# Performance work log

Hardware: AMD Instinct MI355X
Metric: run time of the kernel (lower is better)

## Reference

```python
import jax, jax.numpy as jnp
import numpy as np


def _find(parent, x):
    # chase parent pointers to the root (root = min-rank node of its component)
    return jax.lax.while_loop(lambda v: parent[v] != v, lambda v: parent[v], x)


def _pd0_single(fcol, src, dst):
    """0-dim persistence diagram for one filtration column.

    Semantics match TOGL.generate_persistence_diagram_dim0:
      - nodes are added in sorted order of fcol; birth(node) = its sorted rank
      - directed edge (u, v) merges components at step rank(v) iff rank(u) < rank(v)
      - elder rule: the component whose root has the larger rank dies
      - output row i = (birth=i, death) for the node of rank i (insertion order of
        the original dict is exactly rank order); death = inf for survivors.
    """
    n = fcol.shape[0]
    order = jnp.argsort(fcol)
    rank = jnp.zeros((n,), jnp.int32).at[order].set(jnp.arange(n, dtype=jnp.int32))
    a = rank[src]                      # rank-space endpoints
    b = rank[dst]
    valid = a < b                      # only edges whose source is already active fire
    w = jnp.where(valid, b, n)         # edge weight = step at which it fires
    perm = jnp.argsort(w)              # Kruskal order
    ea, eb, ev = a[perm], b[perm], valid[perm]

    def step(carry, e):
        parent, deaths = carry
        ia, ib, v = e
        ra = _find(parent, ia)
        rb = _find(parent, ib)
        merge = v & (ra != rb)
        elder = jnp.minimum(ra, rb)
        younger = jnp.maximum(ra, rb)
        deaths = deaths.at[younger].set(jnp.where(merge, ib.astype(deaths.dtype), deaths[younger]))
        parent = parent.at[younger].set(jnp.where(merge, elder, parent[younger]))
        # path compression at the two queried nodes
        parent = parent.at[ia].set(jnp.where(merge, elder, ra))
        parent = parent.at[ib].set(jnp.where(merge, elder, rb))
        return (parent, deaths), None

    parent0 = jnp.arange(n, dtype=jnp.int32)
    deaths0 = jnp.full((n,), jnp.inf, jnp.float32)
    (parent, deaths), _ = jax.lax.scan(step, (parent0, deaths0), (ea, eb, ev))
    births = jnp.arange(n, dtype=jnp.float32)
    return jnp.stack([births, deaths], axis=1)  # (n_nodes, 2)


def setup_inputs() -> dict:
    key = jax.random.key(0)
    k = jax.random.split(key, 6)
    N, F, H, NF, E = 20000, 1024, 2048, 4, 160000
    X = jax.random.normal(k[0], (N, F), jnp.float32)
    edge_index = jax.random.randint(k[1], (2, E), 0, N, jnp.int64)
    W1 = jax.random.normal(k[2], (F, H), jnp.float32) / np.sqrt(F)
    b1 = jax.random.normal(k[3], (H,), jnp.float32) * 0.01
    W2 = jax.random.normal(k[4], (H, NF), jnp.float32) / np.sqrt(H)
    b2 = jax.random.normal(k[5], (NF,), jnp.float32) * 0.01
    return {"X": X, "edge_index": edge_index, "W1": W1, "b1": b1, "W2": W2, "b2": b2}


def reference(X, edge_index, W1, b1, W2, b2):
    # filter_graph: Linear -> ReLU -> Linear
    filt = jnp.maximum(X @ W1 + b1, 0.0) @ W2 + b2            # (N, n_filtrations)
    src = edge_index[0].astype(jnp.int32)
    dst = edge_index[1].astype(jnp.int32)
    diagrams = jax.vmap(_pd0_single, in_axes=(1, None, None))(filt, src, dst)  # (NF, N, 2)
    return filt, diagrams
```

## Files before the change

### kernel.cpp

```cpp
#include <hip/hip_runtime.h>

typedef unsigned long long u64;
typedef unsigned int u32;
typedef unsigned short ushort_t;
typedef __attribute__((ext_vector_type(8))) short short8;
typedef __attribute__((ext_vector_type(4))) float fx4;

#define F_DIM 1024
#define H_DIM 2048
#define NFOUT 4
#define WS_W1T_OFF (1ull << 20)
#define WS_XS_OFF  (16ull << 20)
#define PB_BYTES   ((size_t)H_DIM * F_DIM * 2)

__device__ __forceinline__ ushort_t f2bf(float x)
{
    union { float f; u32 u; } c; c.f = x;
    u32 b = c.u;
    u32 r = b + 0x7FFFu + ((b >> 16) & 1u);
    return (ushort_t)(r >> 16);
}
__device__ __forceinline__ float bf2f(ushort_t h)
{
    union { u32 u; float f; } c; c.u = ((u32)h) << 16;
    return c.f;
}
__device__ __forceinline__ void split3(float x, ushort_t& u0, ushort_t& u1, ushort_t& u2)
{
    u0 = f2bf(x);
    float r1 = x - bf2f(u0);
    u1 = f2bf(r1);
    float r2 = r1 - bf2f(u1);
    u2 = f2bf(r2);
}

__device__ __forceinline__ void gload16(const void* g, void* l)
{
    __builtin_amdgcn_global_load_lds(
        (const __attribute__((address_space(1))) unsigned int*)g,
        (__attribute__((address_space(3))) unsigned int*)l, 16, 0, 0);
}

__global__ __launch_bounds__(256)
void k_w1split(const float* __restrict__ W1, ushort_t* __restrict__ w1t)
{
    __shared__ __align__(16) ushort_t LT[3][64][72];
    const int t = threadIdx.x;
    const int bk = blockIdx.x >> 5;
    const int bh = blockIdx.x & 31;
    const int k0 = bk * 64, h0 = bh * 64;
    const int kk = t >> 4, hb = (t & 15) * 4;
    #pragma unroll
    for (int j = 0; j < 4; j++) {
        int row = kk + j * 16;
        float4 v = *(const float4*)(W1 + (size_t)(k0 + row) * H_DIM + h0 + hb);
        float xs[4] = { v.x, v.y, v.z, v.w };
        #pragma unroll
        for (int c = 0; c < 4; c++) {
            ushort_t u0, u1, u2;
            split3(xs[c], u0, u1, u2);
            LT[0][hb + c][row] = u0;
            LT[1][hb + c][row] = u1;
            LT[2][hb + c][row] = u2;
        }
    }
    __syncthreads();
    const int hl = t >> 2, sg = t & 3;
    char* wb = (char*)w1t;
    const int hsw = (hl & 7) << 4;
    #pragma unroll
    for (int p = 0; p < 3; p++)
        #pragma unroll
        for (int q = 0; q < 2; q++) {
            int ks = sg * 16 + q * 8;
            *(short8*)(wb + (size_t)p * PB_BYTES + (size_t)(h0 + hl) * 2048
                       + bk * 128 + ((ks * 2) ^ hsw)) =
                *(const short8*)&LT[p][hl][ks];
        }
}

__global__ __launch_bounds__(256)
void k_xsplit(const float* __restrict__ X, ushort_t* __restrict__ xs,
              int N, int Npad)
{
    const int row = blockIdx.x;
    if (row >= N) return;
    const int t = threadIdx.x;
    float4 v = *(const float4*)(X + (size_t)row * F_DIM + t * 4);
    const int swz = (row & 7) << 4;
    const int off = ((t * 8) & ~127) | (((t * 8) & 127) ^ swz);
    const size_t PA = (size_t)Npad * 2048;
    char* base = (char*)xs + (size_t)row * 2048 + off;
    float in[4] = { v.x, v.y, v.z, v.w };
    ushort4 u0, u1, u2;
    ushort_t* p0 = (ushort_t*)&u0; ushort_t* p1 = (ushort_t*)&u1; ushort_t* p2 = (ushort_t*)&u2;
    #pragma unroll
    for (int j = 0; j < 4; j++) split3(in[j], p0[j], p1[j], p2[j]);
    *(ushort4*)(base)          = u0;
    *(ushort4*)(base + PA)     = u1;
    *(ushort4*)(base + 2 * PA) = u2;
}

__device__ __forceinline__ fx4 mfma16(short8 a, short8 b, fx4 c)
{
    return __builtin_amdgcn_mfma_f32_16x16x32_bf16(a, b, c, 0, 0, 0);
}

#define A4_BYTES (3 * 80 * 128)
#define B4_BYTES (3 * 256 * 128)
#define W24_OFF  (A4_BYTES + B4_BYTES)
#define SM4_BYTES (W24_OFF + 256 * 4 * 4)
#define HP4 260

__global__ __launch_bounds__(512, 1)
void k_filt_mfma4(const ushort_t* __restrict__ xs, const ushort_t* __restrict__ w1t,
                  const float* __restrict__ b1, const float* __restrict__ W2,
                  const float* __restrict__ b2, float* __restrict__ out,
                  int N, int Npad)
{
    extern __shared__ char smem[];
    char* Ac = smem;
    char* Bc = smem + A4_BYTES;
    float* W2s = (float*)(smem + W24_OFF);
    float* hid = (float*)smem;

    const int t = threadIdx.x;
    const int lane = t & 63;
    const int w = t >> 6;
    const int wc = w * 32;
    const int r0 = blockIdx.x * 80;
    const int l15 = lane & 15, l4 = lane >> 4;
    const int fsw = (l15 & 7) << 4;

    const char* xsb = (const char*)xs;
    const char* w1b = (const char*)w1t;
    const size_t PA = (size_t)Npad * 2048;
    const int laneoff = (lane >> 3) * 2048 + ((lane & 7) << 4);

    const int orow = t >> 2;
    const int onf  = t & 3;

    fx4 acc[5][2];
    #pragma unroll
    for (int i = 0; i < 5; i++)
        #pragma unroll
        for (int j = 0; j < 2; j++) acc[i][j] = (fx4)(0.f);
    float pacc = 0.f;

    for (int it = 0; it < 128; ++it) {
        const int hc = it >> 4, kc = it & 15;

        __syncthreads();

        for (int g = w; g < 126; g += 8) {
            char* ldsb; const char* src;
            if (g < 30) {
                const int p = g / 10, rg = g - p * 10;
                ldsb = Ac + p * 10240 + rg * 1024;
                src  = xsb + (size_t)p * PA + (size_t)(r0 + rg * 8) * 2048 + kc * 128;
            } else {
                const int gb = g - 30;
                const int p = gb >> 5, rg = gb & 31;
                ldsb = Bc + p * 32768 + rg * 1024;
                src  = w1b + (size_t)p * PB_BYTES + (size_t)(hc * 256 + rg * 8) * 2048 + kc * 128;
            }
            gload16(src + laneoff, ldsb);
        }
        if (kc == 0 && t < 256)
            *(float4*)&W2s[t * 4] = *(const float4*)(W2 + ((size_t)hc * 256 + t) * NFOUT);

        __syncthreads();

        #pragma unroll
        for (int sub = 0; sub < 2; ++sub) {
            const int kb = (sub * 64 + l4 * 16) ^ fsw;
            short8 b[2][3];
            #pragma unroll
            for (int cf = 0; cf < 2; ++cf) {
                const int hrow = wc + cf * 16 + l15;
                #pragma unroll
                for (int p = 0; p < 3; p++)
                    b[cf][p] = *(const short8*)(Bc + p * 32768 + hrow * 128 + kb);
            }
            #pragma unroll
            for (int rr = 0; rr < 5; ++rr) {
                const int row = rr * 16 + l15;
                short8 a0 = *(const short8*)(Ac + 0 * 10240 + row * 128 + kb);
                short8 a1 = *(const short8*)(Ac + 1 * 10240 + row * 128 + kb);
                short8 a2 = *(const short8*)(Ac + 2 * 10240 + row * 128 + kb);
                #pragma unroll
                for (int cf = 0; cf < 2; ++cf) {
                    fx4 c = acc[rr][cf];
                    c = mfma16(a0, b[cf][0], c);
                    c = mfma16(a0, b[cf][1], c);
                    c = mfma16(a1, b[cf][0], c);
                    c = mfma16(a0, b[cf][2], c);
                    c = mfma16(a1, b[cf][1], c);
                    c = mfma16(a2, b[cf][0], c);
                    acc[rr][cf] = c;
                }
            }
        }

        if (kc == 15) {
            __syncthreads();
            #pragma unroll
            for (int rr = 0; rr < 5; ++rr)
                #pragma unroll
                for (int cf = 0; cf < 2; ++cf) {
                    const int hl = wc + cf * 16 + l15;
                    const float bias1 = b1[hc * 256 + hl];
                    #pragma unroll
                    for (int g = 0; g < 4; g++) {
                        const int rl = rr * 16 + l4 * 4 + g;
                        hid[rl * HP4 + hl] = fmaxf(acc[rr][cf][g] + bias1, 0.f);
                    }
                    acc[rr][cf] = (fx4)(0.f);
                }
            __syncthreads();
            if (orow < 80) {
                const float* hp = hid + orow * HP4;
                #pragma unroll 16
                for (int j = 0; j < 256; j++)
                    pacc = fmaf(hp[j], W2s[j * 4 + onf], pacc);
            }
        }
    }

    if (orow < 80) {
        const int rg = r0 + orow;
        if (rg < N) out[(size_t)rg * NFOUT + onf] = pacc + b2[onf];
    }
}

#define AP_BYTES (3 * 128 * 128)
#define BP_BYTES (3 * 256 * 128)
#define W2_OFF   (AP_BYTES + BP_BYTES)
#define SM_BYTES (W2_OFF + 256 * 4 * 4)
#define HPITCH 260

__global__ __launch_bounds__(512, 2)
void k_filt_mfma3(const float* __restrict__ X, const ushort_t* __restrict__ w1t,
                  const float* __restrict__ b1, const float* __restrict__ W2,
                  const float* __restrict__ b2, float* __restrict__ out, int N)
{
    extern __shared__ char smem[];
    char* Ac = smem;
    char* Bc = smem + AP_BYTES;
    float* W2s = (float*)(smem + W2_OFF);
    float* hid = (float*)smem;

    const int t = threadIdx.x;
    const int lane = t & 63;
    const int w = t >> 6;
    const int wr = (w >> 2) * 64;
    const int wc = (w & 3) * 64;
    const int r0 = blockIdx.x * 128;
    const int l15 = lane & 15, l4 = lane >> 4;
    const int fsw = (l15 & 7) << 4;

    const int arow = t >> 2;
    const int aq   = (t & 3);
    const bool arow_ok = (r0 + arow) < N;
    const int brow = t >> 1;
    const int bseg = (t & 1) * 64;
    const int orow = t >> 2;
    const int onf  = t & 3;

    float Afl[16];
    short8 Bv[12];
    fx4 acc[4][4];
    float pacc = 0.f;
    #pragma unroll
    for (int i = 0; i < 4; i++)
        #pragma unroll
        for (int j = 0; j < 4; j++) acc[i][j] = (fx4)(0.f);

    {
        if (arow_ok) {
            #pragma unroll
            for (int q = 0; q < 4; q++) {
                float4 v = *(const float4*)(X + (size_t)(r0 + arow) * F_DIM + aq * 16 + q * 4);
                Afl[q * 4 + 0] = v.x; Afl[q * 4 + 1] = v.y;
                Afl[q * 4 + 2] = v.z; Afl[q * 4 + 3] = v.w;
            }
        } else {
            #pragma unroll
            for (int j = 0; j < 16; j++) Afl[j] = 0.f;
        }
        #pragma unroll
        for (int p = 0; p < 3; p++)
            #pragma unroll
            for (int q = 0; q < 4; q++)
                Bv[p * 4 + q] = *(const short8*)((const char*)w1t + (size_t)p * PB_BYTES
                                 + (size_t)brow * 2048 + bseg + q * 16);
    }

    for (int it = 0; it < 128; ++it) {
        const int hc = it >> 4, kc = it & 15;

        ushort_t s0[16], s1[16], s2[16];
        #pragma unroll
        for (int j = 0; j < 16; j++) split3(Afl[j], s0[j], s1[j], s2[j]);

        __syncthreads();

        {
            const int aswz = (arow & 7) << 4;
            #pragma unroll
            for (int p = 0; p < 3; p++) {
                const ushort_t* sp = (p == 0) ? s0 : (p == 1) ? s1 : s2;
                #pragma unroll
                for (int h = 0; h < 2; h++) {
                    short8 pk;
                    #pragma unroll
                    for (int i = 0; i < 8; i++) pk[i] = (short)sp[h * 8 + i];
                    *(short8*)(Ac + p * 16384 + arow * 128 + ((aq * 32 + h * 16) ^ aswz)) = pk;
                }
            }
            const int bswz = (brow & 7) << 4;
            #pragma unroll
            for (int p = 0; p < 3; p++)
                #pragma unroll
                for (int q = 0; q < 4; q++)
                    *(short8*)(Bc + p * 32768 + brow * 128 + ((bseg + q * 16) ^ bswz)) = Bv[p * 4 + q];
            if (kc == 0 && t < 256)
                *(float4*)&W2s[t * 4] = *(const float4*)(W2 + ((size_t)hc * 256 + t) * NFOUT);
        }

        if (it + 1 < 128) {
            const int hn = (it + 1) >> 4, kn = (it + 1) & 15;
            if (arow_ok) {
                #pragma unroll
                for (int q = 0; q < 4; q++) {
                    float4 v = *(const float4*)(X + (size_t)(r0 + arow) * F_DIM + kn * 64 + aq * 16 + q * 4);
                    Afl[q * 4 + 0] = v.x; Afl[q * 4 + 1] = v.y;
                    Afl[q * 4 + 2] = v.z; Afl[q * 4 + 3] = v.w;
                }
            }
            #pragma unroll
            for (int p = 0; p < 3; p++)
                #pragma unroll
                for (int q = 0; q < 4; q++)
                    Bv[p * 4 + q] = *(const short8*)((const char*)w1t + (size_t)p * PB_BYTES
                                     + (size_t)(hn * 256 + brow) * 2048 + kn * 128 + bseg + q * 16);
        }

        __syncthreads();

        #pragma unroll
        for (int sub = 0; sub < 2; ++sub) {
            const int kb = sub * 64 + l4 * 16;
            short8 b[4][3];
            #pragma unroll
            for (int cf = 0; cf < 4; ++cf) {
                const int hrow = wc + cf * 16 + l15;
                #pragma unroll
                for (int p = 0; p < 3; p++)
                    b[cf][p] = *(const short8*)(Bc + p * 32768 + hrow * 128 + (kb ^ fsw));
            }
            #pragma unroll
            for (int rr = 0; rr < 4; ++rr) {
                const int row = wr + rr * 16 + l15;
                short8 a0 = *(const short8*)(Ac + 0 * 16384 + row * 128 + (kb ^ fsw));
                short8 a1 = *(const short8*)(Ac + 1 * 16384 + row * 128 + (kb ^ fsw));
                short8 a2 = *(const short8*)(Ac + 2 * 16384 + row * 128 + (kb ^ fsw));
                #pragma unroll
                for (int cf = 0; cf < 4; ++cf) {
                    fx4 c = acc[rr][cf];
                    c = mfma16(a0, b[cf][0], c);
                    c = mfma16(a0, b[cf][1], c);
                    c = mfma16(a1, b[cf][0], c);
                    c = mfma16(a0, b[cf][2], c);
                    c = mfma16(a1, b[cf][1], c);
                    c = mfma16(a2, b[cf][0], c);
                    acc[rr][cf] = c;
                }
            }
        }

        if (kc == 15) {
            __syncthreads();
            #pragma unroll
            for (int rr = 0; rr < 4; ++rr)
                #pragma unroll
                for (int cf = 0; cf < 4; ++cf) {
                    const int hl = wc + cf * 16 + l15;
                    const float bias1 = b1[hc * 256 + hl];
                    #pragma unroll
                    for (int g = 0; g < 4; g++) {
                        const int rl = wr + rr * 16 + l4 * 4 + g;
                        hid[rl * HPITCH + hl] = fmaxf(acc[rr][cf][g] + bias1, 0.f);
                    }
                    acc[rr][cf] = (fx4)(0.f);
                }
            __syncthreads();
            {
                const float* hp = hid + orow * HPITCH;
                #pragma unroll 16
                for (int j = 0; j < 256; j++)
                    pacc = fmaf(hp[j], W2s[j * 4 + onf], pacc);
            }
        }
    }

    {
        const int rg = r0 + orow;
        if (rg < N) out[(size_t)rg * NFOUT + onf] = pacc + b2[onf];
    }
}

#define BM 64
#define BH 64
#define KCH 64
#define LROW 68

__global__ __launch_bounds__(256, 2)
void k_filt(const float* __restrict__ X, const float* __restrict__ W1,
            const float* __restrict__ b1, const float* __restrict__ W2,
            const float* __restrict__ b2, float* __restrict__ out, int N)
{
    __shared__ float Xs[KCH * LROW];
    __shared__ float Ws[KCH * LROW];
    __shared__ float W2s[BH * NFOUT];
    const int t = threadIdx.x;
    const int r0 = blockIdx.x * BM;
    const int tr = t >> 4, tc = t & 15;
    const int orow = t >> 2, onf = t & 3;
    float fchain = 0.0f;
    for (int hc = 0; hc < H_DIM; hc += BH) {
        float acc[4][4];
        #pragma unroll
        for (int i = 0; i < 4; i++)
            #pragma unroll
            for (int j = 0; j < 4; j++) acc[i][j] = 0.0f;
        for (int kc = 0; kc < F_DIM; kc += KCH) {
            {
                const int rowq = t >> 4, kkq = t & 15;
                float xv[4][4];
                #pragma unroll
                for (int j = 0; j < 4; j++) {
                    int r = r0 + rowq * 4 + j;
                    float4 v = (r < N) ? *(const float4*)(X + (size_t)r * F_DIM + kc + kkq * 4)
                                       : make_float4(0.f, 0.f, 0.f, 0.f);
                    xv[j][0] = v.x; xv[j][1] = v.y; xv[j][2] = v.z; xv[j][3] = v.w;
                }
                #pragma unroll
                for (int j = 0; j < 4; j++)
                    *(float4*)&Xs[(kkq * 4 + j) * LROW + rowq * 4] =
                        make_float4(xv[0][j], xv[1][j], xv[2][j], xv[3][j]);
            }
            {
                const int hq = t & 15;
                #pragma unroll
                for (int q = 0; q < 4; q++) {
                    int kk = (t >> 4) + q * 16;
                    *(float4*)&Ws[kk * LROW + hq * 4] =
                        *(const float4*)(W1 + (size_t)(kc + kk) * H_DIM + hc + hq * 4);
                }
            }
            __syncthreads();
            #pragma unroll 8
            for (int kk = 0; kk < KCH; kk++) {
                float4 xv = *(float4*)&Xs[kk * LROW + tr * 4];
                float4 wv = *(float4*)&Ws[kk * LROW + tc * 4];
                acc[0][0] = fmaf(xv.x, wv.x, acc[0][0]); acc[0][1] = fmaf(xv.x, wv.y, acc[0][1]);
                acc[0][2] = fmaf(xv.x, wv.z, acc[0][2]); acc[0][3] = fmaf(xv.x, wv.w, acc[0][3]);
                acc[1][0] = fmaf(xv.y, wv.x, acc[1][0]); acc[1][1] = fmaf(xv.y, wv.y, acc[1][1]);
                acc[1][2] = fmaf(xv.y, wv.z, acc[1][2]); acc[1][3] = fmaf(xv.y, wv.w, acc[1][3]);
                acc[2][0] = fmaf(xv.z, wv.x, acc[2][0]); acc[2][1] = fmaf(xv.z, wv.y, acc[2][1]);
                acc[2][2] = fmaf(xv.z, wv.z, acc[2][2]); acc[2][3] = fmaf(xv.z, wv.w, acc[2][3]);
                acc[3][0] = fmaf(xv.w, wv.x, acc[3][0]); acc[3][1] = fmaf(xv.w, wv.y, acc[3][1]);
                acc[3][2] = fmaf(xv.w, wv.z, acc[3][2]); acc[3][3] = fmaf(xv.w, wv.w, acc[3][3]);
            }
            __syncthreads();
        }
        {
            float4 bv = *(const float4*)(b1 + hc + tc * 4);
            #pragma unroll
            for (int i = 0; i < 4; i++) {
                float4 hv;
                hv.x = fmaxf(acc[i][0] + bv.x, 0.f);
                hv.y = fmaxf(acc[i][1] + bv.y, 0.f);
                hv.z = fmaxf(acc[i][2] + bv.z, 0.f);
                hv.w = fmaxf(acc[i][3] + bv.w, 0.f);
                *(float4*)&Ws[(tr * 4 + i) * LROW + tc * 4] = hv;
            }
            if (t < BH)
                *(float4*)&W2s[t * 4] = *(const float4*)(W2 + (size_t)(hc + t) * NFOUT);
        }
        __syncthreads();
        #pragma unroll 16
        for (int hh = 0; hh < BH; hh++)
            fchain = fmaf(Ws[orow * LROW + hh], W2s[hh * 4 + onf], fchain);
        __syncthreads();
    }
    {
        int r = r0 + orow;
        if (r < N) out[(size_t)r * NFOUT + onf] = fchain + b2[onf];
    }
}

__global__ void k_prep(u32* __restrict__ rank, int N)
{
    int g = blockIdx.x * blockDim.x + threadIdx.x;
    if (g < 4 * N) rank[g] = 0u;
}

#define JTILE 2048

__global__ __launch_bounds__(256)
void k_rank(const float* __restrict__ filt, u32* __restrict__ rank,
            int N, int nchunk)
{
    __shared__ float4 lds[JTILE];
    const int chunk = blockIdx.x % nchunk;
    const int jslice = blockIdx.x / nchunk;
    const int jt = jslice * JTILE;
    const int i = chunk * 256 + threadIdx.x;
    const bool iok = i < N;
    float4 vi = iok ? *(const float4*)(filt + (size_t)i * 4)
                    : make_float4(0.f, 0.f, 0.f, 0.f);
    for (int s = 0; s < JTILE; s += 256) {
        int j = jt + s + threadIdx.x;
        lds[s + threadIdx.x] = (j < N)
            ? *(const float4*)(filt + (size_t)j * 4)
            : make_float4(INFINITY, INFINITY, INFINITY, INFINITY);
    }
    __syncthreads();
    int c0 = 0, c1 = 0, c2 = 0, c3 = 0;
    #pragma unroll 4
    for (int jj = 0; jj < JTILE; jj++) {
        float4 vj = lds[jj];
        int j = jt + jj;
        bool jlt = j < i;
        c0 += (vj.x < vi.x) || (vj.x == vi.x && jlt);
        c1 += (vj.y < vi.y) || (vj.y == vi.y && jlt);
        c2 += (vj.z < vi.z) || (vj.z == vi.z && jlt);
        c3 += (vj.w < vi.w) || (vj.w == vi.w && jlt);
    }
    if (iok) {
        atomicAdd(&rank[0 * N + i], (u32)c0);
        atomicAdd(&rank[1 * N + i], (u32)c1);
        atomicAdd(&rank[2 * N + i], (u32)c2);
        atomicAdd(&rank[3 * N + i], (u32)c3);
    }
}

__device__ __forceinline__ u32 lds_aload(u32* p)
{
    return __hip_atomic_load(p, __ATOMIC_RELAXED, __HIP_MEMORY_SCOPE_WORKGROUP);
}

__device__ __forceinline__ u32 rep_walk32(u32* S, u32 u, u32 t, u32& sv_out)
{
    u32 sv = lds_aload(&S[u]);
    while ((sv >> 16) <= t) {
        u = sv & 0xFFFFu;
        sv = lds_aload(&S[u]);
    }
    sv_out = sv;
    return u;
}

__device__ void do_merge32(u32* S, u32 u, u32 v, u32 t)
{
    for (int guard = 0; guard < (1 << 22); guard++) {
        u32 svu, svv;
        u = rep_walk32(S, u, t, svu);
        v = rep_walk32(S, v, t, svv);
        if (u == v) return;
        if (u < v) { u32 tm = u; u = v; v = tm; u32 ts = svu; svu = svv; svv = ts; }
        u32 s = svu >> 16;
        if (s <= t) continue;
        u32 des = (t << 16) | v;
        u32 old = atomicCAS(&S[u], svu, des);
        if (old == svu) {
            if (s == 0xFFFFu) return;
            u = v; v = old & 0xFFFFu;
            t = s;
        }
    }
}

__global__ __launch_bounds__(1024, 1)
void k_merge4(const int* __restrict__ eidx, const u32* __restrict__ rank,
              float* __restrict__ dg, int N, int E)
{
    extern __shared__ u32 S[];
    const int f = blockIdx.x;
    const u32* rk = rank + (size_t)f * N;

    for (int u = threadIdx.x; u < N; u += blockDim.x)
        S[u] = (0xFFFFu << 16) | (u32)u;
    __syncthreads();

    for (int e = threadIdx.x; e < E; e += blockDim.x) {
        u32 a = rk[eidx[e]];
        u32 b = rk[eidx[E + e]];
        if (a < b) do_merge32(S, a, b, b);
    }
    __syncthreads();

    for (int r = threadIdx.x; r < N; r += blockDim.x) {
        u32 s = S[r] >> 16;
        float death = (s == 0xFFFFu) ? 3.0e38f : (float)s;
        dg[(size_t)f * N * 2 + (size_t)r * 2 + 0] = (float)r;
        dg[(size_t)f * N * 2 + (size_t)r * 2 + 1] = death;
    }
}

extern "C" void kernel_launch(void* const* d_in, const int* in_sizes, int n_in,
                              void* d_out, int out_size, void* d_ws, size_t ws_size,
                              hipStream_t stream)
{
    const float* X  = (const float*)d_in[0];
    const int*   EI = (const int*)d_in[1];
    const float* W1 = (const float*)d_in[2];
    const float* b1 = (const float*)d_in[3];
    const float* W2 = (const float*)d_in[4];
    const float* b2 = (const float*)d_in[5];
    const int N = in_sizes[0] / F_DIM;
    const int E = in_sizes[1] / 2;

    float* out = (float*)d_out;
    float* dg  = out + (size_t)N * NFOUT;
    u32* rank  = (u32*)d_ws;

    static bool attr_set = false;
    if (!attr_set) {
        (void)hipFuncSetAttribute((const void*)k_merge4,
                                  hipFuncAttributeMaxDynamicSharedMemorySize, 160 * 1024);
        (void)hipFuncSetAttribute((const void*)k_filt_mfma3,
                                  hipFuncAttributeMaxDynamicSharedMemorySize, 160 * 1024);
        (void)hipFuncSetAttribute((const void*)k_filt_mfma4,
                                  hipFuncAttributeMaxDynamicSharedMemorySize, 160 * 1024);
        attr_set = true;
    }

    k_prep<<<(4 * N + 255) / 256, 256, 0, stream>>>(rank, N);

    const int Npad = ((N + 79) / 80) * 80;
    const size_t need_w1t = WS_W1T_OFF + 3ull * PB_BYTES;
    const size_t need_xs  = WS_XS_OFF + 3ull * (size_t)Npad * 2048;

    if (ws_size >= need_xs) {
        ushort_t* w1t = (ushort_t*)((char*)d_ws + WS_W1T_OFF);
        ushort_t* xsp = (ushort_t*)((char*)d_ws + WS_XS_OFF);
        k_w1split<<<512, 256, 0, stream>>>(W1, w1t);
        k_xsplit<<<N, 256, 0, stream>>>(X, xsp, N, Npad);
        k_filt_mfma4<<<Npad / 80, 512, SM4_BYTES, stream>>>(xsp, w1t, b1, W2, b2, out, N, Npad);
    } else if (ws_size >= need_w1t) {
        ushort_t* w1t = (ushort_t*)((char*)d_ws + WS_W1T_OFF);
        k_w1split<<<512, 256, 0, stream>>>(W1, w1t);
        k_filt_mfma3<<<(N + 127) / 128, 512, SM_BYTES, stream>>>(X, w1t, b1, W2, b2, out, N);
    } else {
        k_filt<<<(N + BM - 1) / BM, 256, 0, stream>>>(X, W1, b1, W2, b2, out, N);
    }

    const int nchunk = (N + 255) / 256;
    const int njt    = (N + JTILE - 1) / JTILE;
    k_rank<<<nchunk * njt, 256, 0, stream>>>(out, rank, N, nchunk);
    k_merge4<<<4, 1024, (size_t)N * sizeof(u32), stream>>>(EI, rank, dg, N, E);
}
```

Before: 1.457 ms.

## Split K across wave pairs in filter GEMM and bucket merge edges by rank

The bf16x3 filter GEMM kernel now has each pair of waves split the K chunk in half, and each wave computes 64 hidden columns instead of 32. The two partial sums are reduced through LDS before bias and ReLU. Global-to-LDS load addresses are precomputed once outside the main loop, and the launch bound is raised to 2 blocks per CU. The union-find merge kernel now processes edges in 5 passes bucketed by death rank (b>>12), which adds repeated edge reads but may lower contention and deep find chains.

```diff
diff --git a/kernel.cpp b/kernel.cpp
--- a/kernel.cpp
+++ b/kernel.cpp
@@ -106,31 +106,33 @@
     return __builtin_amdgcn_mfma_f32_16x16x32_bf16(a, b, c, 0, 0, 0);
 }
 
-#define A4_BYTES (3 * 80 * 128)
-#define B4_BYTES (3 * 256 * 128)
-#define W24_OFF  (A4_BYTES + B4_BYTES)
-#define SM4_BYTES (W24_OFF + 256 * 4 * 4)
-#define HP4 260
-
-__global__ __launch_bounds__(512, 1)
-void k_filt_mfma4(const ushort_t* __restrict__ xs, const ushort_t* __restrict__ w1t,
+#define A5_BYTES (3 * 80 * 128)
+#define B5_BYTES (3 * 256 * 128)
+#define W25_OFF  (A5_BYTES + B5_BYTES)
+#define SM5_BYTES (W25_OFF + 256 * 4 * 4)
+#define HP5 260
+
+__global__ __launch_bounds__(512, 2)
+void k_filt_mfma5(const ushort_t* __restrict__ xs, const ushort_t* __restrict__ w1t,
                   const float* __restrict__ b1, const float* __restrict__ W2,
                   const float* __restrict__ b2, float* __restrict__ out,
                   int N, int Npad)
 {
     extern __shared__ char smem[];
     char* Ac = smem;
-    char* Bc = smem + A4_BYTES;
-    float* W2s = (float*)(smem + W24_OFF);
+    char* Bc = smem + A5_BYTES;
+    float* W2s = (float*)(smem + W25_OFF);
     float* hid = (float*)smem;
 
     const int t = threadIdx.x;
     const int lane = t & 63;
     const int w = t >> 6;
-    const int wc = w * 32;
+    const int ksub = w & 1;
+    const int wc = (w >> 1) * 64;
     const int r0 = blockIdx.x * 80;
     const int l15 = lane & 15, l4 = lane >> 4;
     const int fsw = (l15 & 7) << 4;
+    const int kb = (ksub * 64 + l4 * 16) ^ fsw;
 
     const char* xsb = (const char*)xs;
     const char* w1b = (const char*)w1t;
@@ -140,11 +142,31 @@
     const int orow = t >> 2;
     const int onf  = t & 3;
 
-    fx4 acc[5][2];
+    const char* srcb[16];
+    char* dstb[16];
+    bool isA[16];
+    #pragma unroll
+    for (int i = 0; i < 16; ++i) {
+        const int g = w + 8 * i;
+        if (g < 30) {
+            const int p = g / 10, rg = g - p * 10;
+            isA[i] = true;
+            dstb[i] = Ac + p * 10240 + rg * 1024;
+            srcb[i] = xsb + (size_t)p * PA + (size_t)(r0 + rg * 8) * 2048 + laneoff;
+        } else {
+            const int gb = g - 30;
+            const int p = gb >> 5, rg = gb & 31;
+            isA[i] = false;
+            dstb[i] = Bc + p * 32768 + rg * 1024;
+            srcb[i] = w1b + (size_t)p * PB_BYTES + (size_t)(rg * 8) * 2048 + laneoff;
+        }
+    }
+
+    fx4 acc[5][4];
     #pragma unroll
     for (int i = 0; i < 5; i++)
         #pragma unroll
-        for (int j = 0; j < 2; j++) acc[i][j] = (fx4)(0.f);
+        for (int j = 0; j < 4; j++) acc[i][j] = (fx4)(0.f);
     float pacc = 0.f;
 
     for (int it = 0; it < 128; ++it) {
@@ -152,35 +174,28 @@
 
         __syncthreads();
 
-        for (int g = w; g < 126; g += 8) {
-            char* ldsb; const char* src;
-            if (g < 30) {
-                const int p = g / 10, rg = g - p * 10;
-                ldsb = Ac + p * 10240 + rg * 1024;
-                src  = xsb + (size_t)p * PA + (size_t)(r0 + rg * 8) * 2048 + kc * 128;
-            } else {
-                const int gb = g - 30;
-                const int p = gb >> 5, rg = gb & 31;
-                ldsb = Bc + p * 32768 + rg * 1024;
-                src  = w1b + (size_t)p * PB_BYTES + (size_t)(hc * 256 + rg * 8) * 2048 + kc * 128;
-            }
-            gload16(src + laneoff, ldsb);
+        {
+            const size_t kcoff = (size_t)(kc * 128);
+            const size_t bcoff = (size_t)hc * 524288 + kcoff;
+            #pragma unroll
+            for (int i = 0; i < 16; ++i) {
+                if (i == 15 && w >= 6) continue;
+                gload16(srcb[i] + (isA[i] ? kcoff : bcoff), dstb[i]);
+            }
         }
         if (kc == 0 && t < 256)
             *(float4*)&W2s[t * 4] = *(const float4*)(W2 + ((size_t)hc * 256 + t) * NFOUT);
 
         __syncthreads();
 
-        #pragma unroll
-        for (int sub = 0; sub < 2; ++sub) {
-            const int kb = (sub * 64 + l4 * 16) ^ fsw;
-            short8 b[2][3];
-            #pragma unroll
-            for (int cf = 0; cf < 2; ++cf) {
+        {
+            short8 bfr[4][3];
+            #pragma unroll
+            for (int cf = 0; cf < 4; ++cf) {
                 const int hrow = wc + cf * 16 + l15;
                 #pragma unroll
                 for (int p = 0; p < 3; p++)
-                    b[cf][p] = *(const short8*)(Bc + p * 32768 + hrow * 128 + kb);
+                    bfr[cf][p] = *(const short8*)(Bc + p * 32768 + hrow * 128 + kb);
             }
             #pragma unroll
             for (int rr = 0; rr < 5; ++rr) {
@@ -189,14 +204,14 @@
                 short8 a1 = *(const short8*)(Ac + 1 * 10240 + row * 128 + kb);
                 short8 a2 = *(const short8*)(Ac + 2 * 10240 + row * 128 + kb);
                 #pragma unroll
-                for (int cf = 0; cf < 2; ++cf) {
+                for (int cf = 0; cf < 4; ++cf) {
                     fx4 c = acc[rr][cf];
-                    c = mfma16(a0, b[cf][0], c);
-                    c = mfma16(a0, b[cf][1], c);
-                    c = mfma16(a1, b[cf][0], c);
-                    c = mfma16(a0, b[cf][2], c);
-                    c = mfma16(a1, b[cf][1], c);
-                    c = mfma16(a2, b[cf][0], c);
+                    c = mfma16(a0, bfr[cf][0], c);
+                    c = mfma16(a0, bfr[cf][1], c);
+                    c = mfma16(a1, bfr[cf][0], c);
+                    c = mfma16(a0, bfr[cf][2], c);
+                    c = mfma16(a1, bfr[cf][1], c);
+                    c = mfma16(a2, bfr[cf][0], c);
                     acc[rr][cf] = c;
                 }
             }
@@ -204,22 +219,40 @@
 
         if (kc == 15) {
             __syncthreads();
-            #pragma unroll
-            for (int rr = 0; rr < 5; ++rr)
-                #pragma unroll
-                for (int cf = 0; cf < 2; ++cf) {
-                    const int hl = wc + cf * 16 + l15;
-                    const float bias1 = b1[hc * 256 + hl];
+            if (ksub == 0) {
+                #pragma unroll
+                for (int rr = 0; rr < 5; ++rr)
                     #pragma unroll
-                    for (int g = 0; g < 4; g++) {
-                        const int rl = rr * 16 + l4 * 4 + g;
-                        hid[rl * HP4 + hl] = fmaxf(acc[rr][cf][g] + bias1, 0.f);
+                    for (int cf = 0; cf < 4; ++cf) {
+                        const int hl = wc + cf * 16 + l15;
+                        #pragma unroll
+                        for (int g = 0; g < 4; g++) {
+                            const int rl = rr * 16 + l4 * 4 + g;
+                            hid[rl * HP5 + hl] = acc[rr][cf][g];
+                        }
+                        acc[rr][cf] = (fx4)(0.f);
                     }
-                    acc[rr][cf] = (fx4)(0.f);
-                }
+            }
             __syncthreads();
-            if (orow < 80) {
-                const float* hp = hid + orow * HP4;
+            if (ksub == 1) {
+                #pragma unroll
+                for (int rr = 0; rr < 5; ++rr)
+                    #pragma unroll
+                    for (int cf = 0; cf < 4; ++cf) {
+                        const int hl = wc + cf * 16 + l15;
+                        const float b1v = b1[hc * 256 + hl];
+                        #pragma unroll
+                        for (int g = 0; g < 4; g++) {
+                            const int rl = rr * 16 + l4 * 4 + g;
+                            hid[rl * HP5 + hl] =
+                                fmaxf(hid[rl * HP5 + hl] + acc[rr][cf][g] + b1v, 0.f);
+                        }
+                        acc[rr][cf] = (fx4)(0.f);
+                    }
+            }
+            __syncthreads();
+            if (t < 320) {
+                const float* hp = hid + orow * HP5;
                 #pragma unroll 16
                 for (int j = 0; j < 256; j++)
                     pacc = fmaf(hp[j], W2s[j * 4 + onf], pacc);
@@ -227,7 +260,7 @@
         }
     }
 
-    if (orow < 80) {
+    if (t < 320) {
         const int rg = r0 + orow;
         if (rg < N) out[(size_t)rg * NFOUT + onf] = pacc + b2[onf];
     }
@@ -595,10 +628,12 @@
         S[u] = (0xFFFFu << 16) | (u32)u;
     __syncthreads();
 
-    for (int e = threadIdx.x; e < E; e += blockDim.x) {
-        u32 a = rk[eidx[e]];
-        u32 b = rk[eidx[E + e]];
-        if (a < b) do_merge32(S, a, b, b);
+    for (int pass = 0; pass < 5; ++pass) {
+        for (int e = threadIdx.x; e < E; e += blockDim.x) {
+            u32 a = rk[eidx[e]];
+            u32 b = rk[eidx[E + e]];
+            if (a < b && (b >> 12) == (u32)pass) do_merge32(S, a, b, b);
+        }
     }
     __syncthreads();
 
@@ -633,7 +668,7 @@
                                   hipFuncAttributeMaxDynamicSharedMemorySize, 160 * 1024);
         (void)hipFuncSetAttribute((const void*)k_filt_mfma3,
                                   hipFuncAttributeMaxDynamicSharedMemorySize, 160 * 1024);
-        (void)hipFuncSetAttribute((const void*)k_filt_mfma4,
+        (void)hipFuncSetAttribute((const void*)k_filt_mfma5,
                                   hipFuncAttributeMaxDynamicSharedMemorySize, 160 * 1024);
         attr_set = true;
     }
@@ -649,7 +684,7 @@
         ushort_t* xsp = (ushort_t*)((char*)d_ws + WS_XS_OFF);
         k_w1split<<<512, 256, 0, stream>>>(W1, w1t);
         k_xsplit<<<N, 256, 0, stream>>>(X, xsp, N, Npad);
-        k_filt_mfma4<<<Npad / 80, 512, SM4_BYTES, stream>>>(xsp, w1t, b1, W2, b2, out, N, Npad);
+        k_filt_mfma5<<<Npad / 80, 512, SM5_BYTES, stream>>>(xsp, w1t, b1, W2, b2, out, N, Npad);
     } else if (ws_size >= need_w1t) {
         ushort_t* w1t = (ushort_t*)((char*)d_ws + WS_W1T_OFF);
         k_w1split<<<512, 256, 0, stream>>>(W1, w1t);
```

Result: slower. 1.871 ms (+28.4%).
